# Optimization experiments

Measured on AMD Instinct MI355X. Metric: run time of the kernel, lower is better.

The kernel has to match this reference:

```python
import jax, jax.numpy as jnp
import numpy as np

N_NODES = 100000
N_EDGES = 600000
N_CLASS = 26
HIDDEN = 128


def setup_inputs() -> dict:
    key = jax.random.key(0)
    ks = jax.random.split(key, 8)
    x = jax.random.normal(ks[0], (N_NODES, N_CLASS), dtype=jnp.float32)
    edge_index = jax.random.randint(ks[1], (2, N_EDGES), 0, N_NODES, dtype=jnp.int64)
    edge_weight = jax.random.uniform(ks[2], (N_EDGES,), dtype=jnp.float32)
    W1 = jax.random.normal(ks[3], (N_CLASS, HIDDEN), dtype=jnp.float32) * (1.0 / np.sqrt(N_CLASS))
    b1 = jnp.zeros((HIDDEN,), dtype=jnp.float32)
    W2 = jax.random.normal(ks[4], (HIDDEN, HIDDEN), dtype=jnp.float32) * (1.0 / np.sqrt(HIDDEN))
    b2 = jnp.zeros((HIDDEN,), dtype=jnp.float32)
    Wfc = jax.random.normal(ks[5], (HIDDEN, N_CLASS), dtype=jnp.float32) * (1.0 / np.sqrt(HIDDEN))
    bfc = jnp.zeros((N_CLASS,), dtype=jnp.float32)
    return {"x": x, "edge_index": edge_index, "edge_weight": edge_weight,
            "W1": W1, "b1": b1, "W2": W2, "b2": b2, "Wfc": Wfc, "bfc": bfc}


def _gcn_norm(edge_index, edge_weight, n_nodes):
    # PyG gcn_norm: add self-loops (weight 1), symmetric deg^-1/2 normalization.
    loop = jnp.arange(n_nodes, dtype=edge_index.dtype)
    row = jnp.concatenate([edge_index[0], loop])  # source
    col = jnp.concatenate([edge_index[1], loop])  # destination
    w = jnp.concatenate([edge_weight, jnp.ones((n_nodes,), edge_weight.dtype)])
    deg = jax.ops.segment_sum(w, col, num_segments=n_nodes)
    d_inv_sqrt = jnp.where(deg > 0, jax.lax.rsqrt(jnp.maximum(deg, 1e-12)), 0.0)
    norm = d_inv_sqrt[row] * w * d_inv_sqrt[col]
    return row, col, norm


def _gcn_conv(x, row, col, norm, W, b, n_nodes):
    h = x @ W                              # [N, out]
    msg = norm[:, None] * h[row]           # gather + scale, [E+N, out]
    out = jax.ops.segment_sum(msg, col, num_segments=n_nodes)  # scatter-add
    return out + b


def reference(x, edge_index, edge_weight, W1, b1, W2, b2, Wfc, bfc):
    n = x.shape[0]
    row, col, norm = _gcn_norm(edge_index, edge_weight, n)
    h = jax.nn.relu(_gcn_conv(x, row, col, norm, W1, b1, n))
    h = jax.nn.relu(_gcn_conv(h, row, col, norm, W2, b2, n))
    return h @ Wfc + bfc
```

## Files before the change

kernel.cpp:

```cpp
#include <hip/hip_runtime.h>

#define NNODES 100000
#define NEDGES 600000
#define NCLASS 26
#define HID    128

#define SHIFT  9
#define BCOLS  512
#define NBKT   196
#define EPB    1024
#define NBE    586
#define NH     (NBKT * NBE)

typedef __attribute__((ext_vector_type(8))) short bf16x8;
typedef __attribute__((ext_vector_type(4))) float f32x4;

__device__ inline unsigned short f2bf(float f) {
    unsigned int u = __float_as_uint(f);
    u += 0x7fffu + ((u >> 16) & 1u);
    return (unsigned short)(u >> 16);
}
__device__ inline unsigned int packbf(float a, float b) {
    return (unsigned int)f2bf(a) | ((unsigned int)f2bf(b) << 16);
}
__device__ inline float2 bfpair(unsigned int p) {
    float2 r;
    r.x = __uint_as_float(p << 16);
    r.y = __uint_as_float(p & 0xffff0000u);
    return r;
}

__global__ __launch_bounds__(256) void histA_k(const int* __restrict__ col,
                                               int* __restrict__ H) {
    __shared__ int h[NBKT];
    int t = threadIdx.x;
    for (int i = t; i < NBKT; i += 256) h[i] = 0;
    __syncthreads();
    int base = blockIdx.x * EPB;
#pragma unroll
    for (int u = 0; u < 4; u++) {
        int e = base + t + u * 256;
        if (e < NEDGES) atomicAdd(&h[col[e] >> SHIFT], 1);
    }
    __syncthreads();
    for (int i = t; i < NBKT; i += 256) H[i * NBE + blockIdx.x] = h[i];
}

__global__ void scanH1_k(const int* __restrict__ in, int* __restrict__ incl,
                         int* __restrict__ aux, int n) {
    __shared__ int s[256];
    int t = threadIdx.x, gi = blockIdx.x * 256 + t;
    s[t] = (gi < n) ? in[gi] : 0;
    __syncthreads();
    for (int off = 1; off < 256; off <<= 1) {
        int x = (t >= off) ? s[t - off] : 0;
        __syncthreads();
        s[t] += x;
        __syncthreads();
    }
    if (gi < n) incl[gi] = s[t];
    if (t == 255) aux[blockIdx.x] = s[255];
}

__global__ void scan2_k(int* __restrict__ aux, int n) {
    __shared__ int s[512];
    int t = threadIdx.x;
    s[t] = (t < n) ? aux[t] : 0;
    __syncthreads();
    for (int off = 1; off < 512; off <<= 1) {
        int x = (t >= off) ? s[t - off] : 0;
        __syncthreads();
        s[t] += x;
        __syncthreads();
    }
    if (t < n) aux[t] = s[t];
}

__device__ inline int exoff(const int* __restrict__ incl, const int* __restrict__ H,
                            const int* __restrict__ aux, int gi) {
    int add = (gi >= 256) ? aux[(gi >> 8) - 1] : 0;
    return incl[gi] - H[gi] + add;
}

__global__ __launch_bounds__(256) void partB_k(const int* __restrict__ row,
                                               const int* __restrict__ col,
                                               const float* __restrict__ w,
                                               const int* __restrict__ incl,
                                               const int* __restrict__ H,
                                               const int* __restrict__ aux,
                                               uint2* __restrict__ rw,
                                               unsigned short* __restrict__ lc) {
    __shared__ int off[NBKT];
    __shared__ int cur[NBKT];
    int t = threadIdx.x;
    for (int i = t; i < NBKT; i += 256) {
        off[i] = exoff(incl, H, aux, i * NBE + blockIdx.x);
        cur[i] = 0;
    }
    __syncthreads();
    int base = blockIdx.x * EPB;
#pragma unroll
    for (int u = 0; u < 4; u++) {
        int e = base + t + u * 256;
        if (e < NEDGES) {
            int c = col[e], b = c >> SHIFT;
            int p = off[b] + atomicAdd(&cur[b], 1);
            rw[p] = make_uint2((unsigned int)row[e], __float_as_uint(w[e]));
            lc[p] = (unsigned short)(c & (BCOLS - 1));
        }
    }
}

__global__ __launch_bounds__(256) void segbp_k(const uint2* __restrict__ rw,
                                               const unsigned short* __restrict__ lc,
                                               const int* __restrict__ incl,
                                               const int* __restrict__ H,
                                               const int* __restrict__ aux,
                                               int* __restrict__ rowptr,
                                               float* __restrict__ dis,
                                               uint2* __restrict__ meta) {
    __shared__ int   cnt[BCOLS];
    __shared__ float ws[BCOLS];
    __shared__ int   rpl[BCOLS];
    __shared__ int   ps[256];
    int b = blockIdx.x, t = threadIdx.x;
    int c0 = b << SHIFT;
    int ncols = min(BCOLS, NNODES - c0);
    for (int i = t; i < BCOLS; i += 256) { cnt[i] = 0; ws[i] = 0.f; }
    __syncthreads();
    int s    = exoff(incl, H, aux, b * NBE);
    int eend = (b == NBKT - 1) ? NEDGES : exoff(incl, H, aux, (b + 1) * NBE);
    for (int e = s + t; e < eend; e += 256) {
        uint2 m = rw[e];
        int l = lc[e];
        atomicAdd(&cnt[l], 1);
        atomicAdd(&ws[l], __uint_as_float(m.y));
    }
    __syncthreads();
    for (int i = t; i < ncols; i += 256) dis[c0 + i] = rsqrtf(1.0f + ws[i]);
    int a0 = cnt[2 * t], a1 = cnt[2 * t + 1];
    ps[t] = a0 + a1;
    __syncthreads();
    for (int off = 1; off < 256; off <<= 1) {
        int x = (t >= off) ? ps[t - off] : 0;
        __syncthreads();
        ps[t] += x;
        __syncthreads();
    }
    int ex = (t > 0) ? ps[t - 1] : 0;
    rpl[2 * t]     = s + ex;
    rpl[2 * t + 1] = s + ex + a0;
    if (2 * t     < ncols) rowptr[c0 + 2 * t]     = s + ex;
    if (2 * t + 1 < ncols) rowptr[c0 + 2 * t + 1] = s + ex + a0;
    if (b == NBKT - 1 && t == 0) rowptr[NNODES] = NEDGES;
    cnt[2 * t] = 0; cnt[2 * t + 1] = 0;
    __syncthreads();
    for (int e = s + t; e < eend; e += 256) {
        uint2 m = rw[e];
        int l = lc[e];
        int pos = rpl[l] + atomicAdd(&cnt[l], 1);
        meta[pos] = make_uint2(m.x, m.y);
    }
}

__global__ __launch_bounds__(256) void prep_k(const float* __restrict__ W2,
                                              const float* __restrict__ W1,
                                              const float* __restrict__ Wfc,
                                              const float* __restrict__ x,
                                              const float* __restrict__ dis,
                                              unsigned short* __restrict__ wt,
                                              unsigned short* __restrict__ w1t,
                                              unsigned short* __restrict__ wfct,
                                              unsigned int* __restrict__ xp) {
    int b = blockIdx.x, t = threadIdx.x;
    if (b < 64) {
        int idx = b * 256 + t;
        int c = idx >> 7, k = idx & 127;
        wt[c * 128 + k] = f2bf(W2[k * 128 + c]);
    } else if (b < 80) {
        int idx = (b - 64) * 256 + t;
        int c = idx >> 5, k = idx & 31;
        w1t[c * 32 + k] = (k < NCLASS) ? f2bf(W1[k * 128 + c]) : (unsigned short)0;
    } else if (b < 96) {
        int idx = (b - 80) * 256 + t;
        int c = idx >> 7, k = idx & 127;
        wfct[c * 128 + k] = (c < NCLASS) ? f2bf(Wfc[k * NCLASS + c]) : (unsigned short)0;
    } else {
        int i = (b - 96) * 256 + t;
        if (i < NNODES * 16) {
            int r = i >> 4, u = i & 15, f0 = u * 2;
            float d = dis[r];
            float a = (f0     < NCLASS) ? x[r * NCLASS + f0]     : 0.f;
            float c = (f0 + 1 < NCLASS) ? x[r * NCLASS + f0 + 1] : 0.f;
            xp[i] = packbf(d * a, d * c);
        }
    }
}

__global__ __launch_bounds__(256) void agg26_k(const int* __restrict__ rowptr,
                                               const uint2* __restrict__ meta,
                                               const unsigned int* __restrict__ xp,
                                               const float* __restrict__ dis,
                                               unsigned int* __restrict__ aggx) {
    int node = blockIdx.x * 16 + (threadIdx.x >> 4);
    int lane = threadIdx.x & 15;

    float2 acc = bfpair(xp[node * 16 + lane]);
    int j = rowptr[node], jend = rowptr[node + 1];
    for (; j + 3 < jend; j += 4) {
        uint2 m0 = meta[j],     m1 = meta[j + 1];
        uint2 m2 = meta[j + 2], m3 = meta[j + 3];
        unsigned int g0 = xp[m0.x * 16 + lane];
        unsigned int g1 = xp[m1.x * 16 + lane];
        unsigned int g2 = xp[m2.x * 16 + lane];
        unsigned int g3 = xp[m3.x * 16 + lane];
        float v0 = __uint_as_float(m0.y), v1 = __uint_as_float(m1.y);
        float v2 = __uint_as_float(m2.y), v3 = __uint_as_float(m3.y);
        float2 a;
        a = bfpair(g0); acc.x = fmaf(v0, a.x, acc.x); acc.y = fmaf(v0, a.y, acc.y);
        a = bfpair(g1); acc.x = fmaf(v1, a.x, acc.x); acc.y = fmaf(v1, a.y, acc.y);
        a = bfpair(g2); acc.x = fmaf(v2, a.x, acc.x); acc.y = fmaf(v2, a.y, acc.y);
        a = bfpair(g3); acc.x = fmaf(v3, a.x, acc.x); acc.y = fmaf(v3, a.y, acc.y);
    }
    for (; j < jend; j++) {
        uint2 m = meta[j];
        float v = __uint_as_float(m.y);
        float2 a = bfpair(xp[m.x * 16 + lane]);
        acc.x = fmaf(v, a.x, acc.x); acc.y = fmaf(v, a.y, acc.y);
    }
    float d = dis[node];
    aggx[node * 16 + lane] = packbf(d * acc.x, d * acc.y);
}

__global__ __launch_bounds__(256) void gemm12_k(const unsigned short* __restrict__ aggx,
                                                const unsigned short* __restrict__ w1t,
                                                const float* __restrict__ b1,
                                                const unsigned short* __restrict__ wt,
                                                const float* __restrict__ dis,
                                                unsigned short* __restrict__ C, int N) {
    __shared__ unsigned short h1s[128 * 136];
    __shared__ unsigned short Ws[128 * 72];
    const int tid  = threadIdx.x;
    const int wave = tid >> 6, lane = tid & 63;
    const int quad = lane >> 4, l16 = lane & 15;
    const int wm = wave >> 1, wn = wave & 1;
    const int row0 = blockIdx.x * 128;

    bf16x8 a1[4], bw1[4];
#pragma unroll
    for (int t = 0; t < 4; t++) {
        int r = row0 + wm * 64 + t * 16 + l16;
        a1[t] = (r < N) ? *(const bf16x8*)&aggx[(size_t)r * 32 + quad * 8]
                        : (bf16x8)(short)0;
        bw1[t] = *(const bf16x8*)&w1t[(wn * 64 + t * 16 + l16) * 32 + quad * 8];
    }
#pragma unroll
    for (int jj = 0; jj < 4; jj++) {
        int idx = tid + jj * 256;
        int r = idx >> 3, ku = idx & 7;
        *(uint4*)&Ws[r * 72 + ku * 8] = *(const uint4*)&wt[(size_t)r * 128 + ku * 8];
    }
    float b1v[4];
#pragma unroll
    for (int tn = 0; tn < 4; tn++) b1v[tn] = b1[wn * 64 + tn * 16 + l16];
#pragma unroll
    for (int tm = 0; tm < 4; tm++) {
#pragma unroll
        for (int tn = 0; tn < 4; tn++) {
            f32x4 hacc = __builtin_amdgcn_mfma_f32_16x16x32_bf16(
                a1[tm], bw1[tn], (f32x4)0.f, 0, 0, 0);
            int rl = wm * 64 + tm * 16 + quad * 4;
            int col = wn * 64 + tn * 16 + l16;
#pragma unroll
            for (int r = 0; r < 4; r++)
                h1s[(rl + r) * 136 + col] = f2bf(fmaxf(hacc[r] + b1v[tn], 0.f));
        }
    }
    __syncthreads();

    f32x4 acc[4][4];
#pragma unroll
    for (int i = 0; i < 4; i++)
#pragma unroll
        for (int j = 0; j < 4; j++) acc[i][j] = (f32x4)0.f;

    for (int c = 0; c < 2; c++) {
        if (c == 1) {
            __syncthreads();
#pragma unroll
            for (int jj = 0; jj < 4; jj++) {
                int idx = tid + jj * 256;
                int r = idx >> 3, ku = idx & 7;
                *(uint4*)&Ws[r * 72 + ku * 8] =
                    *(const uint4*)&wt[(size_t)r * 128 + 64 + ku * 8];
            }
            __syncthreads();
        }
#pragma unroll
        for (int kc = 0; kc < 2; kc++) {
            const int klA = c * 64 + kc * 32 + quad * 8;
            const int klW = kc * 32 + quad * 8;
            bf16x8 af[4], bfr[4];
#pragma unroll
            for (int t = 0; t < 4; t++) {
                af[t]  = *(const bf16x8*)&h1s[(wm * 64 + t * 16 + l16) * 136 + klA];
                bfr[t] = *(const bf16x8*)&Ws[(wn * 64 + t * 16 + l16) * 72 + klW];
            }
#pragma unroll
            for (int tm = 0; tm < 4; tm++)
#pragma unroll
                for (int tn = 0; tn < 4; tn++)
                    acc[tm][tn] = __builtin_amdgcn_mfma_f32_16x16x32_bf16(
                        af[tm], bfr[tn], acc[tm][tn], 0, 0, 0);
        }
    }

#pragma unroll
    for (int tm = 0; tm < 4; tm++) {
        const int rbase = row0 + wm * 64 + tm * 16 + quad * 4;
        float dv[4];
#pragma unroll
        for (int r = 0; r < 4; r++)
            dv[r] = (rbase + r < N) ? dis[rbase + r] : 0.f;
#pragma unroll
        for (int tn = 0; tn < 4; tn++) {
            const int col = wn * 64 + tn * 16 + l16;
#pragma unroll
            for (int r = 0; r < 4; r++) {
                if (rbase + r < N)
                    C[(size_t)(rbase + r) * 128 + col] = f2bf(dv[r] * acc[tm][tn][r]);
            }
        }
    }
}

__global__ __launch_bounds__(256) void aggfc_k(const int* __restrict__ rowptr,
                                               const uint2* __restrict__ meta,
                                               const uint2* __restrict__ h,
                                               const float* __restrict__ dis,
                                               const float* __restrict__ b2,
                                               const unsigned short* __restrict__ wfct,
                                               const float* __restrict__ bfc,
                                               float* __restrict__ out, int N) {
    __shared__ unsigned short h2s[64 * 136];
    const int tid = threadIdx.x;
    const int wv = tid >> 6, lane = tid & 63;
    const int l32 = lane & 31, sub = lane >> 5;
    const int nbase = blockIdx.x * 64;

#pragma unroll 2
    for (int p = 0; p < 8; p++) {
        int r = p * 8 + wv * 2 + sub;
        int node = nbase + r;
        float4 acc = make_float4(0.f, 0.f, 0.f, 0.f);
        float d = 0.f;
        if (node < N) {
            d = dis[node];
            uint2 hcu = h[(size_t)node * 32 + l32];
            float2 h0 = bfpair(hcu.x), h1 = bfpair(hcu.y);
            acc.x = h0.x; acc.y = h0.y; acc.z = h1.x; acc.w = h1.y;
            int j = rowptr[node], jend = rowptr[node + 1];
            for (; j + 3 < jend; j += 4) {
                uint2 m0 = meta[j],     m1 = meta[j + 1];
                uint2 m2 = meta[j + 2], m3 = meta[j + 3];
                uint2 g0 = h[(size_t)m0.x * 32 + l32];
                uint2 g1 = h[(size_t)m1.x * 32 + l32];
                uint2 g2 = h[(size_t)m2.x * 32 + l32];
                uint2 g3 = h[(size_t)m3.x * 32 + l32];
                float v0 = __uint_as_float(m0.y), v1 = __uint_as_float(m1.y);
                float v2 = __uint_as_float(m2.y), v3 = __uint_as_float(m3.y);
                float2 a, b;
                a = bfpair(g0.x); b = bfpair(g0.y);
                acc.x = fmaf(v0, a.x, acc.x); acc.y = fmaf(v0, a.y, acc.y);
                acc.z = fmaf(v0, b.x, acc.z); acc.w = fmaf(v0, b.y, acc.w);
                a = bfpair(g1.x); b = bfpair(g1.y);
                acc.x = fmaf(v1, a.x, acc.x); acc.y = fmaf(v1, a.y, acc.y);
                acc.z = fmaf(v1, b.x, acc.z); acc.w = fmaf(v1, b.y, acc.w);
                a = bfpair(g2.x); b = bfpair(g2.y);
                acc.x = fmaf(v2, a.x, acc.x); acc.y = fmaf(v2, a.y, acc.y);
                acc.z = fmaf(v2, b.x, acc.z); acc.w = fmaf(v2, b.y, acc.w);
                a = bfpair(g3.x); b = bfpair(g3.y);
                acc.x = fmaf(v3, a.x, acc.x); acc.y = fmaf(v3, a.y, acc.y);
                acc.z = fmaf(v3, b.x, acc.z); acc.w = fmaf(v3, b.y, acc.w);
            }
            for (; j < jend; j++) {
                uint2 m = meta[j];
                float v = __uint_as_float(m.y);
                uint2 g = h[(size_t)m.x * 32 + l32];
                float2 a = bfpair(g.x), b = bfpair(g.y);
                acc.x = fmaf(v, a.x, acc.x); acc.y = fmaf(v, a.y, acc.y);
                acc.z = fmaf(v, b.x, acc.z); acc.w = fmaf(v, b.y, acc.w);
            }
        }
        float4 bv = ((const float4*)b2)[l32];
        acc.x = fmaxf(fmaf(d, acc.x, bv.x), 0.f);
        acc.y = fmaxf(fmaf(d, acc.y, bv.y), 0.f);
        acc.z = fmaxf(fmaf(d, acc.z, bv.z), 0.f);
        acc.w = fmaxf(fmaf(d, acc.w, bv.w), 0.f);
        if (node >= N) { acc = make_float4(0.f, 0.f, 0.f, 0.f); }
        *(uint2*)&h2s[r * 136 + l32 * 4] =
            make_uint2(packbf(acc.x, acc.y), packbf(acc.z, acc.w));
    }
    __syncthreads();

    const int q = lane >> 4, m = lane & 15;
    bf16x8 af[4];
#pragma unroll
    for (int ks = 0; ks < 4; ks++)
        af[ks] = *(const bf16x8*)&h2s[(wv * 16 + m) * 136 + ks * 32 + q * 8];

#pragma unroll
    for (int n = 0; n < 2; n++) {
        f32x4 o = (f32x4)0.f;
#pragma unroll
        for (int ks = 0; ks < 4; ks++) {
            bf16x8 bfr = *(const bf16x8*)&wfct[(size_t)(n * 16 + m) * 128 + ks * 32 + q * 8];
            o = __builtin_amdgcn_mfma_f32_16x16x32_bf16(af[ks], bfr, o, 0, 0, 0);
        }
        int col = n * 16 + m;
        if (col < NCLASS) {
            float bv = bfc[col];
            int r0 = nbase + wv * 16 + q * 4;
#pragma unroll
            for (int r = 0; r < 4; r++) {
                if (r0 + r < N)
                    out[(size_t)(r0 + r) * NCLASS + col] = o[r] + bv;
            }
        }
    }
}

extern "C" void kernel_launch(void* const* d_in, const int* in_sizes, int n_in,
                              void* d_out, int out_size, void* d_ws, size_t ws_size,
                              hipStream_t stream) {
    const float* x   = (const float*)d_in[0];
    const int*   ei  = (const int*)d_in[1];
    const float* ew  = (const float*)d_in[2];
    const float* W1  = (const float*)d_in[3];
    const float* b1  = (const float*)d_in[4];
    const float* W2  = (const float*)d_in[5];
    const float* b2  = (const float*)d_in[6];
    const float* Wfc = (const float*)d_in[7];
    const float* bfc = (const float*)d_in[8];
    float* out = (float*)d_out;

    const int N = NNODES;
    const int* erow = ei;
    const int* ecol = ei + NEDGES;

    float* fws    = (float*)d_ws;
    float* dis    = fws;
    int*   rowptr = (int*)(fws + 100000);
    int*   H      = (int*)(fws + 200004);
    int*   incl   = (int*)(fws + 314860);
    int*   aux    = (int*)(fws + 429716);
    uint2* rw     = (uint2*)(fws + 430228);
    unsigned short* lc = (unsigned short*)(fws + 1630228);
    uint2* meta   = (uint2*)(fws + 1930228);
    unsigned short* wt16   = (unsigned short*)(fws + 3130228);
    unsigned short* w1t16  = (unsigned short*)(fws + 3138420);
    unsigned short* wfct16 = (unsigned short*)(fws + 3140468);
    unsigned int*   xp     = (unsigned int*)(fws + 3142516);
    unsigned int*   aggx   = (unsigned int*)(fws + 4742516);
    unsigned short* hB16   = (unsigned short*)(fws + 6342516);

    const int gScan = (NH + 255) / 256;
    const int g128  = (N + 127) / 128;
    const int gA26  = N / 16;
    const int gPrep = 96 + (N * 16 + 255) / 256;
    const int gFc   = (N + 63) / 64;

    histA_k<<<NBE, 256, 0, stream>>>(ecol, H);
    scanH1_k<<<gScan, 256, 0, stream>>>(H, incl, aux, NH);
    scan2_k<<<1, 512, 0, stream>>>(aux, gScan);
    partB_k<<<NBE, 256, 0, stream>>>(erow, ecol, ew, incl, H, aux, rw, lc);
    segbp_k<<<NBKT, 256, 0, stream>>>(rw, lc, incl, H, aux, rowptr, dis, meta);

    prep_k<<<gPrep, 256, 0, stream>>>(W2, W1, Wfc, x, dis, wt16, w1t16, wfct16, xp);

    agg26_k<<<gA26, 256, 0, stream>>>(rowptr, meta, xp, dis, aggx);
    gemm12_k<<<g128, 256, 0, stream>>>((const unsigned short*)aggx, w1t16, b1,
                                       wt16, dis, hB16, N);

    aggfc_k<<<gFc, 256, 0, stream>>>(rowptr, meta, (const uint2*)hB16, dis, b2,
                                     wfct16, bfc, out, N);
}
```

Before: 209.6 us.

## Fold prep kernel into partition kernels and retile layer GEMM to 64 rows

Removes the separate prep kernel: the weight transposes and bf16 conversions run as extra blocks appended to the partition kernel, and the scaled, packed x features are produced inside the segment kernel right after the degree normalisation is computed. This saves one launch and a re-read of dis. The fused GEMM kernel is restructured to 64-row tiles with one wave per 16 rows, and it reads W2 fragments directly from global memory instead of staging them in shared memory. That cuts shared memory use and doubles the grid, at the cost of more redundant global loads of W2. The segment kernel now does strided x reads over only 196 blocks, which may serialise that work.

Result: slower. 228.5 us (+9.0%).

```diff
diff --git a/kernel.cpp b/kernel.cpp
--- a/kernel.cpp
+++ b/kernel.cpp
@@ -89,10 +89,33 @@
                                                const int* __restrict__ H,
                                                const int* __restrict__ aux,
                                                uint2* __restrict__ rw,
-                                               unsigned short* __restrict__ lc) {
+                                               unsigned short* __restrict__ lc,
+                                               const float* __restrict__ W2,
+                                               const float* __restrict__ W1,
+                                               const float* __restrict__ Wfc,
+                                               unsigned short* __restrict__ wt,
+                                               unsigned short* __restrict__ w1t,
+                                               unsigned short* __restrict__ wfct) {
     __shared__ int off[NBKT];
     __shared__ int cur[NBKT];
     int t = threadIdx.x;
+    if (blockIdx.x >= NBE) {
+        int b = blockIdx.x - NBE;
+        if (b < 64) {
+            int idx = b * 256 + t;
+            int c = idx >> 7, k = idx & 127;
+            wt[c * 128 + k] = f2bf(W2[k * 128 + c]);
+        } else if (b < 80) {
+            int idx = (b - 64) * 256 + t;
+            int c = idx >> 5, k = idx & 31;
+            w1t[c * 32 + k] = (k < NCLASS) ? f2bf(W1[k * 128 + c]) : (unsigned short)0;
+        } else {
+            int idx = (b - 80) * 256 + t;
+            int c = idx >> 7, k = idx & 127;
+            wfct[c * 128 + k] = (c < NCLASS) ? f2bf(Wfc[k * NCLASS + c]) : (unsigned short)0;
+        }
+        return;
+    }
     for (int i = t; i < NBKT; i += 256) {
         off[i] = exoff(incl, H, aux, i * NBE + blockIdx.x);
         cur[i] = 0;
@@ -116,8 +139,10 @@
                                                const int* __restrict__ incl,
                                                const int* __restrict__ H,
                                                const int* __restrict__ aux,
+                                               const float* __restrict__ x,
                                                int* __restrict__ rowptr,
                                                float* __restrict__ dis,
+                                               unsigned int* __restrict__ xp,
                                                uint2* __restrict__ meta) {
     __shared__ int   cnt[BCOLS];
     __shared__ float ws[BCOLS];
@@ -138,13 +163,21 @@
     }
     __syncthreads();
     for (int i = t; i < ncols; i += 256) dis[c0 + i] = rsqrtf(1.0f + ws[i]);
+    for (int i = t; i < ncols * 16; i += 256) {
+        int r = i >> 4, u = i & 15, f0 = u * 2;
+        int node = c0 + r;
+        float d = rsqrtf(1.0f + ws[r]);
+        float a = (f0     < NCLASS) ? x[(size_t)node * NCLASS + f0]     : 0.f;
+        float c = (f0 + 1 < NCLASS) ? x[(size_t)node * NCLASS + f0 + 1] : 0.f;
+        xp[node * 16 + u] = packbf(d * a, d * c);
+    }
     int a0 = cnt[2 * t], a1 = cnt[2 * t + 1];
     ps[t] = a0 + a1;
     __syncthreads();
     for (int off = 1; off < 256; off <<= 1) {
-        int x = (t >= off) ? ps[t - off] : 0;
-        __syncthreads();
-        ps[t] += x;
+        int x2 = (t >= off) ? ps[t - off] : 0;
+        __syncthreads();
+        ps[t] += x2;
         __syncthreads();
     }
     int ex = (t > 0) ? ps[t - 1] : 0;
@@ -160,40 +193,6 @@
         int l = lc[e];
         int pos = rpl[l] + atomicAdd(&cnt[l], 1);
         meta[pos] = make_uint2(m.x, m.y);
-    }
-}
-
-__global__ __launch_bounds__(256) void prep_k(const float* __restrict__ W2,
-                                              const float* __restrict__ W1,
-                                              const float* __restrict__ Wfc,
-                                              const float* __restrict__ x,
-                                              const float* __restrict__ dis,
-                                              unsigned short* __restrict__ wt,
-                                              unsigned short* __restrict__ w1t,
-                                              unsigned short* __restrict__ wfct,
-                                              unsigned int* __restrict__ xp) {
-    int b = blockIdx.x, t = threadIdx.x;
-    if (b < 64) {
-        int idx = b * 256 + t;
-        int c = idx >> 7, k = idx & 127;
-        wt[c * 128 + k] = f2bf(W2[k * 128 + c]);
-    } else if (b < 80) {
-        int idx = (b - 64) * 256 + t;
-        int c = idx >> 5, k = idx & 31;
-        w1t[c * 32 + k] = (k < NCLASS) ? f2bf(W1[k * 128 + c]) : (unsigned short)0;
-    } else if (b < 96) {
-        int idx = (b - 80) * 256 + t;
-        int c = idx >> 7, k = idx & 127;
-        wfct[c * 128 + k] = (c < NCLASS) ? f2bf(Wfc[k * NCLASS + c]) : (unsigned short)0;
-    } else {
-        int i = (b - 96) * 256 + t;
-        if (i < NNODES * 16) {
-            int r = i >> 4, u = i & 15, f0 = u * 2;
-            float d = dis[r];
-            float a = (f0     < NCLASS) ? x[r * NCLASS + f0]     : 0.f;
-            float c = (f0 + 1 < NCLASS) ? x[r * NCLASS + f0 + 1] : 0.f;
-            xp[i] = packbf(d * a, d * c);
-        }
     }
 }
 
@@ -238,98 +237,54 @@
                                                 const unsigned short* __restrict__ wt,
                                                 const float* __restrict__ dis,
                                                 unsigned short* __restrict__ C, int N) {
-    __shared__ unsigned short h1s[128 * 136];
-    __shared__ unsigned short Ws[128 * 72];
+    __shared__ unsigned short h1s[64 * 136];
     const int tid  = threadIdx.x;
-    const int wave = tid >> 6, lane = tid & 63;
+    const int wv = tid >> 6, lane = tid & 63;
     const int quad = lane >> 4, l16 = lane & 15;
-    const int wm = wave >> 1, wn = wave & 1;
-    const int row0 = blockIdx.x * 128;
-
-    bf16x8 a1[4], bw1[4];
-#pragma unroll
-    for (int t = 0; t < 4; t++) {
-        int r = row0 + wm * 64 + t * 16 + l16;
-        a1[t] = (r < N) ? *(const bf16x8*)&aggx[(size_t)r * 32 + quad * 8]
-                        : (bf16x8)(short)0;
-        bw1[t] = *(const bf16x8*)&w1t[(wn * 64 + t * 16 + l16) * 32 + quad * 8];
-    }
-#pragma unroll
-    for (int jj = 0; jj < 4; jj++) {
-        int idx = tid + jj * 256;
-        int r = idx >> 3, ku = idx & 7;
-        *(uint4*)&Ws[r * 72 + ku * 8] = *(const uint4*)&wt[(size_t)r * 128 + ku * 8];
-    }
-    float b1v[4];
-#pragma unroll
-    for (int tn = 0; tn < 4; tn++) b1v[tn] = b1[wn * 64 + tn * 16 + l16];
-#pragma unroll
-    for (int tm = 0; tm < 4; tm++) {
-#pragma unroll
-        for (int tn = 0; tn < 4; tn++) {
-            f32x4 hacc = __builtin_amdgcn_mfma_f32_16x16x32_bf16(
-                a1[tm], bw1[tn], (f32x4)0.f, 0, 0, 0);
-            int rl = wm * 64 + tm * 16 + quad * 4;
-            int col = wn * 64 + tn * 16 + l16;
+    const int row0 = blockIdx.x * 64;
+    const int wrow = wv * 16;
+
+    {
+        int ar = row0 + wrow + l16;
+        bf16x8 af1 = (ar < N) ? *(const bf16x8*)&aggx[(size_t)ar * 32 + quad * 8]
+                              : (bf16x8)(short)0;
+#pragma unroll
+        for (int n = 0; n < 8; n++) {
+            bf16x8 bw = *(const bf16x8*)&w1t[(n * 16 + l16) * 32 + quad * 8];
+            f32x4 hacc = __builtin_amdgcn_mfma_f32_16x16x32_bf16(af1, bw, (f32x4)0.f, 0, 0, 0);
+            int col = n * 16 + l16;
+            float bv = b1[col];
 #pragma unroll
             for (int r = 0; r < 4; r++)
-                h1s[(rl + r) * 136 + col] = f2bf(fmaxf(hacc[r] + b1v[tn], 0.f));
-        }
-    }
-    __syncthreads();
-
-    f32x4 acc[4][4];
-#pragma unroll
-    for (int i = 0; i < 4; i++)
-#pragma unroll
-        for (int j = 0; j < 4; j++) acc[i][j] = (f32x4)0.f;
-
-    for (int c = 0; c < 2; c++) {
-        if (c == 1) {
-            __syncthreads();
-#pragma unroll
-            for (int jj = 0; jj < 4; jj++) {
-                int idx = tid + jj * 256;
-                int r = idx >> 3, ku = idx & 7;
-                *(uint4*)&Ws[r * 72 + ku * 8] =
-                    *(const uint4*)&wt[(size_t)r * 128 + 64 + ku * 8];
-            }
-            __syncthreads();
-        }
-#pragma unroll
-        for (int kc = 0; kc < 2; kc++) {
-            const int klA = c * 64 + kc * 32 + quad * 8;
-            const int klW = kc * 32 + quad * 8;
-            bf16x8 af[4], bfr[4];
-#pragma unroll
-            for (int t = 0; t < 4; t++) {
-                af[t]  = *(const bf16x8*)&h1s[(wm * 64 + t * 16 + l16) * 136 + klA];
-                bfr[t] = *(const bf16x8*)&Ws[(wn * 64 + t * 16 + l16) * 72 + klW];
-            }
-#pragma unroll
-            for (int tm = 0; tm < 4; tm++)
-#pragma unroll
-                for (int tn = 0; tn < 4; tn++)
-                    acc[tm][tn] = __builtin_amdgcn_mfma_f32_16x16x32_bf16(
-                        af[tm], bfr[tn], acc[tm][tn], 0, 0, 0);
-        }
-    }
-
-#pragma unroll
-    for (int tm = 0; tm < 4; tm++) {
-        const int rbase = row0 + wm * 64 + tm * 16 + quad * 4;
-        float dv[4];
-#pragma unroll
-        for (int r = 0; r < 4; r++)
-            dv[r] = (rbase + r < N) ? dis[rbase + r] : 0.f;
-#pragma unroll
-        for (int tn = 0; tn < 4; tn++) {
-            const int col = wn * 64 + tn * 16 + l16;
-#pragma unroll
-            for (int r = 0; r < 4; r++) {
-                if (rbase + r < N)
-                    C[(size_t)(rbase + r) * 128 + col] = f2bf(dv[r] * acc[tm][tn][r]);
-            }
+                h1s[(wrow + quad * 4 + r) * 136 + col] = f2bf(fmaxf(hacc[r] + bv, 0.f));
+        }
+    }
+    __syncthreads();
+
+    bf16x8 af[4];
+#pragma unroll
+    for (int kc = 0; kc < 4; kc++)
+        af[kc] = *(const bf16x8*)&h1s[(wrow + l16) * 136 + kc * 32 + quad * 8];
+
+    const int rbase = row0 + wrow + quad * 4;
+    float dv[4];
+#pragma unroll
+    for (int r = 0; r < 4; r++)
+        dv[r] = (rbase + r < N) ? dis[rbase + r] : 0.f;
+
+#pragma unroll
+    for (int n = 0; n < 8; n++) {
+        f32x4 acc = (f32x4)0.f;
+#pragma unroll
+        for (int kc = 0; kc < 4; kc++) {
+            bf16x8 bfr = *(const bf16x8*)&wt[(size_t)(n * 16 + l16) * 128 + kc * 32 + quad * 8];
+            acc = __builtin_amdgcn_mfma_f32_16x16x32_bf16(af[kc], bfr, acc, 0, 0, 0);
+        }
+        int col = n * 16 + l16;
+#pragma unroll
+        for (int r = 0; r < 4; r++) {
+            if (rbase + r < N)
+                C[(size_t)(rbase + r) * 128 + col] = f2bf(dv[r] * acc[r]);
         }
     }
 }
@@ -465,23 +420,20 @@
     unsigned short* hB16   = (unsigned short*)(fws + 6342516);
 
     const int gScan = (NH + 255) / 256;
-    const int g128  = (N + 127) / 128;
     const int gA26  = N / 16;
-    const int gPrep = 96 + (N * 16 + 255) / 256;
-    const int gFc   = (N + 63) / 64;
+    const int g64   = (N + 63) / 64;
 
     histA_k<<<NBE, 256, 0, stream>>>(ecol, H);
     scanH1_k<<<gScan, 256, 0, stream>>>(H, incl, aux, NH);
     scan2_k<<<1, 512, 0, stream>>>(aux, gScan);
-    partB_k<<<NBE, 256, 0, stream>>>(erow, ecol, ew, incl, H, aux, rw, lc);
-    segbp_k<<<NBKT, 256, 0, stream>>>(rw, lc, incl, H, aux, rowptr, dis, meta);
-
-    prep_k<<<gPrep, 256, 0, stream>>>(W2, W1, Wfc, x, dis, wt16, w1t16, wfct16, xp);
+    partB_k<<<NBE + 96, 256, 0, stream>>>(erow, ecol, ew, incl, H, aux, rw, lc,
+                                          W2, W1, Wfc, wt16, w1t16, wfct16);
+    segbp_k<<<NBKT, 256, 0, stream>>>(rw, lc, incl, H, aux, x, rowptr, dis, xp, meta);
 
     agg26_k<<<gA26, 256, 0, stream>>>(rowptr, meta, xp, dis, aggx);
-    gemm12_k<<<g128, 256, 0, stream>>>((const unsigned short*)aggx, w1t16, b1,
-                                       wt16, dis, hB16, N);
-
-    aggfc_k<<<gFc, 256, 0, stream>>>(rowptr, meta, (const uint2*)hB16, dis, b2,
+    gemm12_k<<<g64, 256, 0, stream>>>((const unsigned short*)aggx, w1t16, b1,
+                                      wt16, dis, hB16, N);
+
+    aggfc_k<<<g64, 256, 0, stream>>>(rowptr, meta, (const uint2*)hB16, dis, b2,
                                      wfct16, bfc, out, N);
 }
```
